# Optimization experiments

Measured on AMD Instinct MI355X. Metric: run time of the kernel, lower is better.

The kernel has to match this reference:

```python
import jax, jax.numpy as jnp
import numpy as np

BN_EPS = 1e-5
N_OUT, D_OUT = 64, 128


def setup_inputs() -> dict:
    key = jax.random.key(0)
    k1, k2, k3, k4 = jax.random.split(key, 4)
    B, N_in, D_in, K = 512, 64, 128, 4
    x = jax.random.normal(k1, (B, N_in, D_in), dtype=jnp.float32)
    # block-sparse weights: one (D_in x D_out) block per (output-row, active-input-row) pair
    W = jax.random.normal(k2, (N_OUT, K, D_in, D_OUT), dtype=jnp.float32) * (1.0 / np.sqrt(K * D_in))
    bias = jax.random.normal(k3, (N_OUT, D_OUT), dtype=jnp.float32) * 0.02
    gamma = jnp.ones((N_OUT * D_OUT,), dtype=jnp.float32)
    beta = jnp.zeros((N_OUT * D_OUT,), dtype=jnp.float32)
    idx = jax.random.randint(k4, (N_OUT, K), 0, N_in, dtype=jnp.int32)
    return {"x": x, "W": W, "bias": bias, "gamma": gamma, "beta": beta, "idx": idx}


def reference(x, W, bias, gamma, beta, idx):
    B = x.shape[0]
    # structured-sparse linear: gather active input rows, per-block matmul
    xg = x[:, idx, :]                                   # [B, N_out, K, D_in]
    y = jnp.einsum('bokd,okde->boe', xg, W) + bias      # [B, N_out, D_out]
    # BatchNorm1d (training-mode batch statistics) on flattened features
    yf = y.reshape(B, -1)                               # [B, N_out*D_out]
    mean = jnp.mean(yf, axis=0)
    var = jnp.mean(jnp.square(yf - mean), axis=0)       # biased variance, as in torch BN
    yn = (yf - mean) * jax.lax.rsqrt(var + BN_EPS) * gamma + beta
    # Swish: z * sigmoid(z)
    out = yn * jax.nn.sigmoid(yn)
    return out.reshape(B, N_OUT, D_OUT)
```

## Files before the change

kernel.cpp:

```cpp
#include <hip/hip_runtime.h>


typedef __attribute__((ext_vector_type(8))) __bf16 bf16x8;
typedef __attribute__((ext_vector_type(4))) float  f32x4;

#define FEAT 8192
#define XROW 8192
#define LDSB 520
#define NX8  524288
#define ADEPTH 6

__global__ __launch_bounds__(256)
void cvt_kernel(const float* __restrict__ x, __bf16* __restrict__ xb)
{
    const int stride = gridDim.x * blockDim.x;
    for (int c = blockIdx.x * blockDim.x + threadIdx.x; c < NX8; c += stride) {
        const f32x4 v0 = *(const f32x4*)(x + c * 8);
        const f32x4 v1 = *(const f32x4*)(x + c * 8 + 4);
        bf16x8 o;
#pragma unroll
        for (int j = 0; j < 4; ++j) {
            o[j]     = (__bf16)v0[j];
            o[j + 4] = (__bf16)v1[j];
        }
        *(bf16x8*)(xb + c * 8) = o;
    }
}

__global__ __launch_bounds__(1024, 4)
void fused_encoder(const __bf16* __restrict__ xb, const float* __restrict__ W,
                   const float* __restrict__ bias, const float* __restrict__ gamma,
                   const float* __restrict__ beta, const int* __restrict__ idxp,
                   float* __restrict__ out)
{
    __shared__ __bf16 Bpan[32 * LDSB];
    __shared__ float Sred[16][32];
    __shared__ float Qred[16][32];
    __shared__ float sscale[32];
    __shared__ float sshift[32];

    const int bid = blockIdx.x;
    const int o   = ((bid >> 5) << 3) | (bid & 7);
    const int es  = (bid >> 3) & 3;
    const int e0  = es * 32;

    const int tid  = threadIdx.x;
    const int wave = tid >> 6;
    const int lane = tid & 63;
    const int lam  = lane & 15;
    const int quad = lane >> 4;

    int rsel[4];
#pragma unroll
    for (int k = 0; k < 4; ++k) rsel[k] = idxp[o * 4 + k];

    const __bf16* xrow0 = xb + (wave * 32 + lam)      * XROW;
    const __bf16* xrow1 = xb + (wave * 32 + 16 + lam) * XROW;

    bf16x8 sa[ADEPTH][2];

    auto loadA = [&](const int stg, const int kkc) {
        const int r  = rsel[kkc >> 2];
        const int dd = (kkc & 3) * 32 + quad * 8;
        sa[stg][0] = *(const bf16x8*)(xrow0 + r * 128 + dd);
        sa[stg][1] = *(const bf16x8*)(xrow1 + r * 128 + dd);
    };

#pragma unroll
    for (int p = 0; p < ADEPTH; ++p) loadA(p, p);

    {
        const int e  = tid & 31;
        const int k0 = (tid >> 5) * 16;
        float v[16];
#pragma unroll
        for (int j = 0; j < 16; ++j) {
            const int k = k0 + j;
            v[j] = W[(((o * 4 + (k >> 7)) * 128) + (k & 127)) * 128 + e0 + e];
        }
        bf16x8 w0, w1;
#pragma unroll
        for (int j = 0; j < 8; ++j) {
            w0[j] = (__bf16)v[j];
            w1[j] = (__bf16)v[8 + j];
        }
        *(bf16x8*)&Bpan[e * LDSB + k0]     = w0;
        *(bf16x8*)&Bpan[e * LDSB + k0 + 8] = w1;
    }

    const f32x4 zero4 = {0.f, 0.f, 0.f, 0.f};
    f32x4 acc[2][2];
#pragma unroll
    for (int mi = 0; mi < 2; ++mi)
#pragma unroll
        for (int ni = 0; ni < 2; ++ni) acc[mi][ni] = zero4;

    __syncthreads();

    bf16x8 bq[2][2];
    bq[0][0] = *(const bf16x8*)&Bpan[lam        * LDSB + quad * 8];
    bq[0][1] = *(const bf16x8*)&Bpan[(16 + lam) * LDSB + quad * 8];

#pragma unroll
    for (int kk = 0; kk < 16; ++kk) {
        const int cur = kk & 1;
        const int stg = kk % ADEPTH;
        if (kk + 1 < 16) {
            bq[cur ^ 1][0] = *(const bf16x8*)&Bpan[lam        * LDSB + (kk + 1) * 32 + quad * 8];
            bq[cur ^ 1][1] = *(const bf16x8*)&Bpan[(16 + lam) * LDSB + (kk + 1) * 32 + quad * 8];
        }
        acc[0][0] = __builtin_amdgcn_mfma_f32_16x16x32_bf16(sa[stg][0], bq[cur][0], acc[0][0], 0, 0, 0);
        acc[0][1] = __builtin_amdgcn_mfma_f32_16x16x32_bf16(sa[stg][0], bq[cur][1], acc[0][1], 0, 0, 0);
        acc[1][0] = __builtin_amdgcn_mfma_f32_16x16x32_bf16(sa[stg][1], bq[cur][0], acc[1][0], 0, 0, 0);
        acc[1][1] = __builtin_amdgcn_mfma_f32_16x16x32_bf16(sa[stg][1], bq[cur][1], acc[1][1], 0, 0, 0);
        if (kk + ADEPTH < 16) loadA(stg, kk + ADEPTH);
    }

    float bvals[2];
#pragma unroll
    for (int ni = 0; ni < 2; ++ni)
        bvals[ni] = bias[o * 128 + e0 + ni * 16 + lam];
#pragma unroll
    for (int mi = 0; mi < 2; ++mi)
#pragma unroll
        for (int ni = 0; ni < 2; ++ni)
#pragma unroll
            for (int rr = 0; rr < 4; ++rr) acc[mi][ni][rr] += bvals[ni];

#pragma unroll
    for (int ni = 0; ni < 2; ++ni) {
        float s = 0.f, q = 0.f;
#pragma unroll
        for (int mi = 0; mi < 2; ++mi)
#pragma unroll
            for (int rr = 0; rr < 4; ++rr) {
                const float v = acc[mi][ni][rr];
                s += v; q += v * v;
            }
        s += __shfl_xor(s, 16); s += __shfl_xor(s, 32);
        q += __shfl_xor(q, 16); q += __shfl_xor(q, 32);
        if (quad == 0) {
            Sred[wave][ni * 16 + lam] = s;
            Qred[wave][ni * 16 + lam] = q;
        }
    }
    __syncthreads();

    if (tid < 32) {
        float s = 0.f, q = 0.f;
#pragma unroll
        for (int w = 0; w < 16; ++w) {
            s += Sred[w][tid];
            q += Qred[w][tid];
        }
        const float mean = s * (1.0f / 512.0f);
        const float var  = q * (1.0f / 512.0f) - mean * mean;
        const float rstd = rsqrtf(var + 1e-5f);
        const float sc   = rstd * gamma[o * 128 + e0 + tid];
        sscale[tid] = sc;
        sshift[tid] = beta[o * 128 + e0 + tid] - mean * sc;
    }
    __syncthreads();

#pragma unroll
    for (int mi = 0; mi < 2; ++mi) {
        const int rowb = wave * 32 + mi * 16 + quad * 4;
#pragma unroll
        for (int ni = 0; ni < 2; ++ni) {
            const int col = ni * 16 + lam;
            const float sc = sscale[col];
            const float sh = sshift[col];
#pragma unroll
            for (int rr = 0; rr < 4; ++rr) {
                const float xn = acc[mi][ni][rr] * sc + sh;
                const float sg = 1.0f / (1.0f + __expf(-xn));
                out[(rowb + rr) * FEAT + o * 128 + e0 + col] = xn * sg;
            }
        }
    }
}

extern "C" void kernel_launch(void* const* d_in, const int* in_sizes, int n_in,
                              void* d_out, int out_size, void* d_ws, size_t ws_size,
                              hipStream_t stream)
{
    const float* x     = (const float*)d_in[0];
    const float* W     = (const float*)d_in[1];
    const float* bias  = (const float*)d_in[2];
    const float* gamma = (const float*)d_in[3];
    const float* beta  = (const float*)d_in[4];
    const int*   idx   = (const int*)d_in[5];
    float* out = (float*)d_out;

    __bf16* xb = (__bf16*)d_ws;

    cvt_kernel<<<dim3(512), dim3(256), 0, stream>>>(x, xb);
    fused_encoder<<<dim3(256), dim3(1024), 0, stream>>>(
        xb, W, bias, gamma, beta, idx, out);
}
```

Before: 106.2 us.

## Pad bf16 x rows and stagger per-wave K order to spread memory accesses

The conversion kernel now writes bf16 x with a padded row stride (8320 instead of 8192 elements), so rows that are a power-of-two apart no longer map to the same memory channels. The fused kernel also rotates the K-chunk start per wave, so different waves read different rows of x and different LDS columns at the same time. Both aim to cut channel and bank conflicts on the gathered A loads and on the B panel reads. In exchange, the row index is now picked through runtime selects, and the workspace needs slightly more space.

```diff
diff --git a/kernel.cpp b/kernel.cpp
--- a/kernel.cpp
+++ b/kernel.cpp
@@ -5,7 +5,7 @@
 typedef __attribute__((ext_vector_type(4))) float  f32x4;
 
 #define FEAT 8192
-#define XROW 8192
+#define XROWP 8320
 #define LDSB 520
 #define NX8  524288
 #define ADEPTH 6
@@ -15,15 +15,17 @@
 {
     const int stride = gridDim.x * blockDim.x;
     for (int c = blockIdx.x * blockDim.x + threadIdx.x; c < NX8; c += stride) {
+        const int b = c >> 10;
+        const int j = c & 1023;
         const f32x4 v0 = *(const f32x4*)(x + c * 8);
         const f32x4 v1 = *(const f32x4*)(x + c * 8 + 4);
         bf16x8 o;
 #pragma unroll
-        for (int j = 0; j < 4; ++j) {
-            o[j]     = (__bf16)v0[j];
-            o[j + 4] = (__bf16)v1[j];
-        }
-        *(bf16x8*)(xb + c * 8) = o;
+        for (int jj = 0; jj < 4; ++jj) {
+            o[jj]     = (__bf16)v0[jj];
+            o[jj + 4] = (__bf16)v1[jj];
+        }
+        *(bf16x8*)(xb + (size_t)b * XROWP + j * 8) = o;
     }
 }
 
@@ -50,24 +52,34 @@
     const int lam  = lane & 15;
     const int quad = lane >> 4;
 
-    int rsel[4];
-#pragma unroll
-    for (int k = 0; k < 4; ++k) rsel[k] = idxp[o * 4 + k];
-
-    const __bf16* xrow0 = xb + (wave * 32 + lam)      * XROW;
-    const __bf16* xrow1 = xb + (wave * 32 + 16 + lam) * XROW;
+    const int r0 = idxp[o * 4 + 0];
+    const int r1 = idxp[o * 4 + 1];
+    const int r2 = idxp[o * 4 + 2];
+    const int r3 = idxp[o * 4 + 3];
+
+    const __bf16* xrow0 = xb + (size_t)(wave * 32 + lam)      * XROWP;
+    const __bf16* xrow1 = xb + (size_t)(wave * 32 + 16 + lam) * XROWP;
+
+    auto rowOf = [&](const int kc) -> int {
+        const int kidx = kc >> 2;
+        const int ra = (kidx & 1) ? r1 : r0;
+        const int rb = (kidx & 1) ? r3 : r2;
+        return (kidx & 2) ? rb : ra;
+    };
 
     bf16x8 sa[ADEPTH][2];
-
-    auto loadA = [&](const int stg, const int kkc) {
-        const int r  = rsel[kkc >> 2];
-        const int dd = (kkc & 3) * 32 + quad * 8;
-        sa[stg][0] = *(const bf16x8*)(xrow0 + r * 128 + dd);
-        sa[stg][1] = *(const bf16x8*)(xrow1 + r * 128 + dd);
+    auto loadA = [&](bf16x8& F0, bf16x8& F1, const int kc) {
+        const int r  = rowOf(kc);
+        const int dd = (kc & 3) * 32 + quad * 8;
+        F0 = *(const bf16x8*)(xrow0 + r * 128 + dd);
+        F1 = *(const bf16x8*)(xrow1 + r * 128 + dd);
     };
 
-#pragma unroll
-    for (int p = 0; p < ADEPTH; ++p) loadA(p, p);
+    const int kk0 = wave;
+
+#pragma unroll
+    for (int p = 0; p < ADEPTH; ++p)
+        loadA(sa[p][0], sa[p][1], (kk0 + p) & 15);
 
     {
         const int e  = tid & 31;
@@ -98,22 +110,24 @@
     __syncthreads();
 
     bf16x8 bq[2][2];
-    bq[0][0] = *(const bf16x8*)&Bpan[lam        * LDSB + quad * 8];
-    bq[0][1] = *(const bf16x8*)&Bpan[(16 + lam) * LDSB + quad * 8];
-
-#pragma unroll
-    for (int kk = 0; kk < 16; ++kk) {
-        const int cur = kk & 1;
-        const int stg = kk % ADEPTH;
-        if (kk + 1 < 16) {
-            bq[cur ^ 1][0] = *(const bf16x8*)&Bpan[lam        * LDSB + (kk + 1) * 32 + quad * 8];
-            bq[cur ^ 1][1] = *(const bf16x8*)&Bpan[(16 + lam) * LDSB + (kk + 1) * 32 + quad * 8];
+    bq[0][0] = *(const bf16x8*)&Bpan[lam        * LDSB + kk0 * 32 + quad * 8];
+    bq[0][1] = *(const bf16x8*)&Bpan[(16 + lam) * LDSB + kk0 * 32 + quad * 8];
+
+#pragma unroll
+    for (int i = 0; i < 16; ++i) {
+        const int cur = i & 1;
+        const int stg = i % ADEPTH;
+        if (i + 1 < 16) {
+            const int kn = (kk0 + i + 1) & 15;
+            bq[cur ^ 1][0] = *(const bf16x8*)&Bpan[lam        * LDSB + kn * 32 + quad * 8];
+            bq[cur ^ 1][1] = *(const bf16x8*)&Bpan[(16 + lam) * LDSB + kn * 32 + quad * 8];
         }
         acc[0][0] = __builtin_amdgcn_mfma_f32_16x16x32_bf16(sa[stg][0], bq[cur][0], acc[0][0], 0, 0, 0);
         acc[0][1] = __builtin_amdgcn_mfma_f32_16x16x32_bf16(sa[stg][0], bq[cur][1], acc[0][1], 0, 0, 0);
         acc[1][0] = __builtin_amdgcn_mfma_f32_16x16x32_bf16(sa[stg][1], bq[cur][0], acc[1][0], 0, 0, 0);
         acc[1][1] = __builtin_amdgcn_mfma_f32_16x16x32_bf16(sa[stg][1], bq[cur][1], acc[1][1], 0, 0, 0);
-        if (kk + ADEPTH < 16) loadA(stg, kk + ADEPTH);
+        if (i + ADEPTH < 16)
+            loadA(sa[stg][0], sa[stg][1], (kk0 + i + ADEPTH) & 15);
     }
 
     float bvals[2];
```

Result: no change. 105.9 us (-0.4%).
